# Kernel tuning notes

Hardware: AMD Instinct MI355X
Metric: run time of the kernel (lower is better)

The kernel has to match this reference:

```python
import jax, jax.numpy as jnp
import numpy as np

B, N_VAR, N_CLAUSE, K = 256, 10000, 40000, 3
N_NODE = N_VAR + N_CLAUSE


def setup_inputs() -> dict:
    key = jax.random.key(0)
    k1, k2, k3 = jax.random.split(key, 3)
    out = jax.random.normal(k1, (B, N_NODE), dtype=jnp.float32)
    # binary labels (torch y are 0/1 floats)
    y = (jax.random.uniform(k2, (B, N_NODE)) > 0.5).astype(jnp.float32)
    # mask: 0 on variable nodes, 1 on clause nodes
    mask = jnp.concatenate(
        [jnp.zeros((B, N_VAR), jnp.float32), jnp.ones((B, N_CLAUSE), jnp.float32)],
        axis=1,
    )
    # clauses: per graph, n_clause clauses of K variable indices in [0, n_var)
    clauses = jax.random.randint(k3, (B, N_CLAUSE, K), 0, N_VAR, dtype=jnp.int32)
    return {
        "out": out,
        "y": y,
        "mask": mask,
        "clauses": clauses,
        "n_var": N_VAR,
        "n_clause": N_CLAUSE,
    }


def _bce_with_logits(x, t):
    # elementwise BCE-with-logits: softplus(x) - x*t (numerically stable)
    return jax.nn.softplus(x) - x * t


def reference(out, y, mask, clauses, n_var, n_clause):
    b = out.shape[0]
    # loss 1: mean BCE over masked logits, divided by n_clause (per graph)
    loss1 = jnp.mean(_bce_with_logits(out * mask, y), axis=1) / n_clause  # [B]

    # hard predictions (detached in torch): sigmoid > 0.5, keep clause nodes only
    pred = (jax.nn.sigmoid(jax.lax.stop_gradient(out)) > 0.5).astype(out.dtype) * mask
    clause_active = pred[:, n_var:]  # [B, n_clause]

    # loadUnsatVariables: for each active clause, set its variables to 1.
    # Order-independent -> scatter-max of clause activation onto variable slots.
    flat_idx = (jnp.arange(b, dtype=jnp.int32)[:, None, None] * n_var
                + clauses).reshape(-1)  # [B*n_clause*K]
    vals = jnp.broadcast_to(clause_active[:, :, None], clauses.shape).reshape(-1)
    var_target = (jnp.zeros(b * n_var, out.dtype)
                  .at[flat_idx].max(vals)
                  .reshape(b, n_var))
    # target * (1 - mask): variable positions keep scatter result, clause part -> 0
    target = jnp.concatenate(
        [var_target, jnp.zeros((b, clause_active.shape[1]), out.dtype)], axis=1)

    loss2 = jnp.mean(_bce_with_logits(out * (1.0 - mask), target), axis=1) * 2.0
    return jnp.sum(loss1 + loss2)
```

## Files before the change

### kernel.cpp

```cpp
#include <hip/hip_runtime.h>

#define BB      256
#define NVAR    10000
#define NCLAUSE 40000
#define NNODE   50000
#define NT      1024


__device__ __forceinline__ float softplusf(float x) {
    return fmaxf(x, 0.f) + __logf(1.f + __expf(-fabsf(x)));
}

__global__ __launch_bounds__(NT) void k_fused(const float* __restrict__ outp,
                                              const float* __restrict__ yp,
                                              const int*   __restrict__ cl,
                                              float* __restrict__ accum) {
    __shared__ unsigned char flags[NVAR];
    __shared__ float red[NT / 64];
    const int b = blockIdx.x;
    const int tid = threadIdx.x;

    unsigned* fw = (unsigned*)flags;
    for (int i = tid; i < NVAR / 4; i += NT) fw[i] = 0u;
    __syncthreads();

    float s1 = 0.f;
    {
        const float* orow = outp + (size_t)b * NNODE + NVAR;
        const float* yrow = yp   + (size_t)b * NNODE + NVAR;
        const int*   crow = cl   + (size_t)b * NCLAUSE * 3;
        for (int t = tid; t < NCLAUSE / 4; t += NT) {
            const float4 o4 = *(const float4*)(orow + 4 * t);
            const float4 y4 = *(const float4*)(yrow + 4 * t);
            const int4* cp = (const int4*)(crow + 12 * t);
            const int4 c0 = cp[0], c1 = cp[1], c2 = cp[2];

            s1 += softplusf(o4.x) - o4.x * y4.x;
            s1 += softplusf(o4.y) - o4.y * y4.y;
            s1 += softplusf(o4.z) - o4.z * y4.z;
            s1 += softplusf(o4.w) - o4.w * y4.w;

            if (o4.x > 0.f) { flags[c0.x] = 1; flags[c0.y] = 1; flags[c0.z] = 1; }
            if (o4.y > 0.f) { flags[c0.w] = 1; flags[c1.x] = 1; flags[c1.y] = 1; }
            if (o4.z > 0.f) { flags[c1.z] = 1; flags[c1.w] = 1; flags[c2.x] = 1; }
            if (o4.w > 0.f) { flags[c2.y] = 1; flags[c2.z] = 1; flags[c2.w] = 1; }
        }
    }
    __syncthreads();

    float s2 = 0.f;
    {
        const float* vrow = outp + (size_t)b * NNODE;
        for (int t = tid; t < NVAR / 4; t += NT) {
            const float4 o4 = *(const float4*)(vrow + 4 * t);
            const unsigned f = fw[t];
            s2 += softplusf(o4.x) - o4.x * (float)( f        & 1u);
            s2 += softplusf(o4.y) - o4.y * (float)((f >> 8)  & 1u);
            s2 += softplusf(o4.z) - o4.z * (float)((f >> 16) & 1u);
            s2 += softplusf(o4.w) - o4.w * (float)((f >> 24) & 1u);
        }
    }

    float v = s1 * (1.0f / ((float)NNODE * (float)NCLAUSE)) + s2 * (2.0f / (float)NNODE);
    #pragma unroll
    for (int off = 32; off; off >>= 1) v += __shfl_down(v, off, 64);
    const int lane = tid & 63, w = tid >> 6;
    if (lane == 0) red[w] = v;
    __syncthreads();
    if (w == 0) {
        float r = (lane < NT / 64) ? red[lane] : 0.f;
        #pragma unroll
        for (int off = 8; off; off >>= 1) r += __shfl_down(r, off, 64);
        if (lane == 0) atomicAdd(accum, r);
    }
}

__global__ void k_fin(const float* __restrict__ accum, float* __restrict__ outp) {
    if (threadIdx.x == 0 && blockIdx.x == 0) {
        const double ln2 = 0.6931471805599453;
        double r = (double)accum[0]
                 + ((double)BB * NVAR * ln2) / ((double)NNODE * (double)NCLAUSE)
                 + 2.0 * ((double)BB * NCLAUSE * ln2) / (double)NNODE;
        outp[0] = (float)r;
    }
}

extern "C" void kernel_launch(void* const* d_in, const int* in_sizes, int n_in,
                              void* d_out, int out_size, void* d_ws, size_t ws_size,
                              hipStream_t stream) {
    const float* outp = (const float*)d_in[0];
    const float* yp   = (const float*)d_in[1];
    const int* cl     = (const int*)d_in[3];

    float* accum = (float*)d_ws;
    hipMemsetAsync(d_ws, 0, 16, stream);

    k_fused<<<BB, NT, 0, stream>>>(outp, yp, cl, accum);
    k_fin<<<1, 64, 0, stream>>>(accum, (float*)d_out);
}
```

Measured before the change: 43.60 us.

## Split clause scatter across two blocks per graph and add separate variable-loss kernel

```diff
diff --git a/kernel.cpp b/kernel.cpp
--- a/kernel.cpp
+++ b/kernel.cpp
@@ -4,32 +4,39 @@
 #define NVAR    10000
 #define NCLAUSE 40000
 #define NNODE   50000
-#define NT      1024
+#define NSPLIT  2
+#define NTA     1024
+#define NTB     512
+#define CL_PER_H (NCLAUSE / NSPLIT)
+#define V4_PER_H (CL_PER_H / 4)
+#define NWORDS   313
+#define LDSW     2504
 
 
 __device__ __forceinline__ float softplusf(float x) {
     return fmaxf(x, 0.f) + __logf(1.f + __expf(-fabsf(x)));
 }
 
-__global__ __launch_bounds__(NT) void k_fused(const float* __restrict__ outp,
-                                              const float* __restrict__ yp,
-                                              const int*   __restrict__ cl,
-                                              float* __restrict__ accum) {
-    __shared__ unsigned char flags[NVAR];
-    __shared__ float red[NT / 64];
-    const int b = blockIdx.x;
+__global__ __launch_bounds__(NTA) void k_clause(const float* __restrict__ outp,
+                                                const float* __restrict__ yp,
+                                                const int*   __restrict__ cl,
+                                                unsigned*    __restrict__ flagw,
+                                                float*       __restrict__ accum) {
+    __shared__ unsigned fw[LDSW];
+    __shared__ float red[NTA / 64];
+    const int b = blockIdx.y, h = blockIdx.x;
     const int tid = threadIdx.x;
 
-    unsigned* fw = (unsigned*)flags;
-    for (int i = tid; i < NVAR / 4; i += NT) fw[i] = 0u;
+    for (int i = tid; i < LDSW; i += NTA) fw[i] = 0u;
     __syncthreads();
 
+    unsigned char* flags = (unsigned char*)fw;
     float s1 = 0.f;
     {
-        const float* orow = outp + (size_t)b * NNODE + NVAR;
-        const float* yrow = yp   + (size_t)b * NNODE + NVAR;
-        const int*   crow = cl   + (size_t)b * NCLAUSE * 3;
-        for (int t = tid; t < NCLAUSE / 4; t += NT) {
+        const float* orow = outp + (size_t)b * NNODE + NVAR + h * CL_PER_H;
+        const float* yrow = yp   + (size_t)b * NNODE + NVAR + h * CL_PER_H;
+        const int*   crow = cl   + (size_t)b * NCLAUSE * 3 + (size_t)h * CL_PER_H * 3;
+        for (int t = tid; t < V4_PER_H; t += NTA) {
             const float4 o4 = *(const float4*)(orow + 4 * t);
             const float4 y4 = *(const float4*)(yrow + 4 * t);
             const int4* cp = (const int4*)(crow + 12 * t);
@@ -48,29 +55,67 @@
     }
     __syncthreads();
 
-    float s2 = 0.f;
-    {
-        const float* vrow = outp + (size_t)b * NNODE;
-        for (int t = tid; t < NVAR / 4; t += NT) {
-            const float4 o4 = *(const float4*)(vrow + 4 * t);
-            const unsigned f = fw[t];
-            s2 += softplusf(o4.x) - o4.x * (float)( f        & 1u);
-            s2 += softplusf(o4.y) - o4.y * (float)((f >> 8)  & 1u);
-            s2 += softplusf(o4.z) - o4.z * (float)((f >> 16) & 1u);
-            s2 += softplusf(o4.w) - o4.w * (float)((f >> 24) & 1u);
+    unsigned* dst = flagw + (size_t)(b * NSPLIT + h) * NWORDS;
+    for (int w = tid; w < NWORDS; w += NTA) {
+        unsigned r = 0;
+        #pragma unroll
+        for (int k = 0; k < 8; ++k) {
+            const unsigned u = fw[w * 8 + k];
+            const unsigned nib = (u | (u >> 7) | (u >> 14) | (u >> 21)) & 0xFu;
+            r |= nib << (4 * k);
         }
+        dst[w] = r;
     }
 
-    float v = s1 * (1.0f / ((float)NNODE * (float)NCLAUSE)) + s2 * (2.0f / (float)NNODE);
+    float v = s1 * (1.0f / ((float)NNODE * (float)NCLAUSE));
     #pragma unroll
     for (int off = 32; off; off >>= 1) v += __shfl_down(v, off, 64);
     const int lane = tid & 63, w = tid >> 6;
     if (lane == 0) red[w] = v;
     __syncthreads();
     if (w == 0) {
-        float r = (lane < NT / 64) ? red[lane] : 0.f;
+        float r = (lane < NTA / 64) ? red[lane] : 0.f;
         #pragma unroll
         for (int off = 8; off; off >>= 1) r += __shfl_down(r, off, 64);
+        if (lane == 0) atomicAdd(accum, r);
+    }
+}
+
+__global__ __launch_bounds__(NTB) void k_var(const float* __restrict__ outp,
+                                             const unsigned* __restrict__ flagw,
+                                             float* __restrict__ accum) {
+    __shared__ unsigned comb[NWORDS];
+    __shared__ float red[NTB / 64];
+    const int b = blockIdx.y, h = blockIdx.x;
+    const int tid = threadIdx.x;
+
+    const unsigned* p0 = flagw + (size_t)(b * NSPLIT + 0) * NWORDS;
+    const unsigned* p1 = flagw + (size_t)(b * NSPLIT + 1) * NWORDS;
+    for (int i = tid; i < NWORDS; i += NTB) comb[i] = p0[i] | p1[i];
+    __syncthreads();
+
+    float s2 = 0.f;
+    const float* vrow = outp + (size_t)b * NNODE + h * (NVAR / NSPLIT);
+    for (int t = tid; t < NVAR / NSPLIT / 4; t += NTB) {
+        const int vt = h * (NVAR / NSPLIT / 4) + t;
+        const float4 o4 = *(const float4*)(vrow + 4 * t);
+        const unsigned bits = (comb[vt >> 3] >> ((4 * vt) & 31)) & 0xFu;
+        s2 += softplusf(o4.x) - o4.x * (float)( bits       & 1u);
+        s2 += softplusf(o4.y) - o4.y * (float)((bits >> 1) & 1u);
+        s2 += softplusf(o4.z) - o4.z * (float)((bits >> 2) & 1u);
+        s2 += softplusf(o4.w) - o4.w * (float)((bits >> 3) & 1u);
+    }
+
+    float v = s2 * (2.0f / (float)NNODE);
+    #pragma unroll
+    for (int off = 32; off; off >>= 1) v += __shfl_down(v, off, 64);
+    const int lane = tid & 63, w = tid >> 6;
+    if (lane == 0) red[w] = v;
+    __syncthreads();
+    if (w == 0) {
+        float r = (lane < NTB / 64) ? red[lane] : 0.f;
+        #pragma unroll
+        for (int off = 4; off; off >>= 1) r += __shfl_down(r, off, 64);
         if (lane == 0) atomicAdd(accum, r);
     }
 }
@@ -93,8 +138,14 @@
     const int* cl     = (const int*)d_in[3];
 
     float* accum = (float*)d_ws;
+    unsigned* flagw = (unsigned*)((char*)d_ws + 16);
     hipMemsetAsync(d_ws, 0, 16, stream);
 
-    k_fused<<<BB, NT, 0, stream>>>(outp, yp, cl, accum);
+    dim3 gA(NSPLIT, BB);
+    k_clause<<<gA, NTA, 0, stream>>>(outp, yp, cl, flagw, accum);
+
+    dim3 gB(NSPLIT, BB);
+    k_var<<<gB, NTB, 0, stream>>>(outp, flagw, accum);
+
     k_fin<<<1, 64, 0, stream>>>(accum, (float*)d_out);
 }
```

After: 51.80 us. 18.8% more time.

## Software-pipeline clause loads, branchless flag stores, fold finalize into last block

Applied to the files above, without the earlier changes.

```diff
diff --git a/kernel.cpp b/kernel.cpp
--- a/kernel.cpp
+++ b/kernel.cpp
@@ -5,59 +5,81 @@
 #define NCLAUSE 40000
 #define NNODE   50000
 #define NT      1024
+#define NV4C    (NCLAUSE / 4)
+#define NV4V    (NVAR / 4)
+#define LDSW    2504
 
 
 __device__ __forceinline__ float softplusf(float x) {
     return fmaxf(x, 0.f) + __logf(1.f + __expf(-fabsf(x)));
 }
 
-__global__ __launch_bounds__(NT) void k_fused(const float* __restrict__ outp,
-                                              const float* __restrict__ yp,
-                                              const int*   __restrict__ cl,
-                                              float* __restrict__ accum) {
-    __shared__ unsigned char flags[NVAR];
+__global__ __launch_bounds__(NT) void k_all(const float* __restrict__ outp,
+                                            const float* __restrict__ yp,
+                                            const int*   __restrict__ cl,
+                                            float* __restrict__ accum,
+                                            unsigned* __restrict__ counter,
+                                            float* __restrict__ res) {
+    __shared__ unsigned fw[LDSW];
     __shared__ float red[NT / 64];
     const int b = blockIdx.x;
     const int tid = threadIdx.x;
+    unsigned char* flags = (unsigned char*)fw;
 
-    unsigned* fw = (unsigned*)flags;
-    for (int i = tid; i < NVAR / 4; i += NT) fw[i] = 0u;
+    for (int i = tid; i < LDSW; i += NT) fw[i] = 0u;
     __syncthreads();
 
+    const float* orow = outp + (size_t)b * NNODE + NVAR;
+    const float* yrow = yp   + (size_t)b * NNODE + NVAR;
+    const int*   crow = cl   + (size_t)b * NCLAUSE * 3;
+
     float s1 = 0.f;
-    {
-        const float* orow = outp + (size_t)b * NNODE + NVAR;
-        const float* yrow = yp   + (size_t)b * NNODE + NVAR;
-        const int*   crow = cl   + (size_t)b * NCLAUSE * 3;
-        for (int t = tid; t < NCLAUSE / 4; t += NT) {
-            const float4 o4 = *(const float4*)(orow + 4 * t);
-            const float4 y4 = *(const float4*)(yrow + 4 * t);
-            const int4* cp = (const int4*)(crow + 12 * t);
-            const int4 c0 = cp[0], c1 = cp[1], c2 = cp[2];
+    int t = tid;
+    bool valid = (t < NV4C);
+    float4 o4, y4; int4 c0, c1, c2;
+    if (valid) {
+        o4 = *(const float4*)(orow + 4 * t);
+        y4 = *(const float4*)(yrow + 4 * t);
+        const int4* cp = (const int4*)(crow + 12 * t);
+        c0 = cp[0]; c1 = cp[1]; c2 = cp[2];
+    }
+    while (valid) {
+        const int tn = t + NT;
+        const bool vn = (tn < NV4C);
+        float4 on, yn; int4 n0, n1, n2;
+        if (vn) {
+            on = *(const float4*)(orow + 4 * tn);
+            yn = *(const float4*)(yrow + 4 * tn);
+            const int4* cp = (const int4*)(crow + 12 * tn);
+            n0 = cp[0]; n1 = cp[1]; n2 = cp[2];
+        }
 
-            s1 += softplusf(o4.x) - o4.x * y4.x;
-            s1 += softplusf(o4.y) - o4.y * y4.y;
-            s1 += softplusf(o4.z) - o4.z * y4.z;
-            s1 += softplusf(o4.w) - o4.w * y4.w;
+        s1 += softplusf(o4.x) - o4.x * y4.x;
+        s1 += softplusf(o4.y) - o4.y * y4.y;
+        s1 += softplusf(o4.z) - o4.z * y4.z;
+        s1 += softplusf(o4.w) - o4.w * y4.w;
 
-            if (o4.x > 0.f) { flags[c0.x] = 1; flags[c0.y] = 1; flags[c0.z] = 1; }
-            if (o4.y > 0.f) { flags[c0.w] = 1; flags[c1.x] = 1; flags[c1.y] = 1; }
-            if (o4.z > 0.f) { flags[c1.z] = 1; flags[c1.w] = 1; flags[c2.x] = 1; }
-            if (o4.w > 0.f) { flags[c2.y] = 1; flags[c2.z] = 1; flags[c2.w] = 1; }
-        }
+        const bool ax = o4.x > 0.f, ay = o4.y > 0.f, az = o4.z > 0.f, aw = o4.w > 0.f;
+        flags[ax ? c0.x : NVAR] = 1; flags[ax ? c0.y : NVAR] = 1; flags[ax ? c0.z : NVAR] = 1;
+        flags[ay ? c0.w : NVAR] = 1; flags[ay ? c1.x : NVAR] = 1; flags[ay ? c1.y : NVAR] = 1;
+        flags[az ? c1.z : NVAR] = 1; flags[az ? c1.w : NVAR] = 1; flags[az ? c2.x : NVAR] = 1;
+        flags[aw ? c2.y : NVAR] = 1; flags[aw ? c2.z : NVAR] = 1; flags[aw ? c2.w : NVAR] = 1;
+
+        t = tn; valid = vn;
+        o4 = on; y4 = yn; c0 = n0; c1 = n1; c2 = n2;
     }
     __syncthreads();
 
     float s2 = 0.f;
     {
         const float* vrow = outp + (size_t)b * NNODE;
-        for (int t = tid; t < NVAR / 4; t += NT) {
-            const float4 o4 = *(const float4*)(vrow + 4 * t);
-            const unsigned f = fw[t];
-            s2 += softplusf(o4.x) - o4.x * (float)( f        & 1u);
-            s2 += softplusf(o4.y) - o4.y * (float)((f >> 8)  & 1u);
-            s2 += softplusf(o4.z) - o4.z * (float)((f >> 16) & 1u);
-            s2 += softplusf(o4.w) - o4.w * (float)((f >> 24) & 1u);
+        for (int v = tid; v < NV4V; v += NT) {
+            const float4 q4 = *(const float4*)(vrow + 4 * v);
+            const unsigned f = fw[v];
+            s2 += softplusf(q4.x) - q4.x * (float)( f        & 1u);
+            s2 += softplusf(q4.y) - q4.y * (float)((f >> 8)  & 1u);
+            s2 += softplusf(q4.z) - q4.z * (float)((f >> 16) & 1u);
+            s2 += softplusf(q4.w) - q4.w * (float)((f >> 24) & 1u);
         }
     }
 
@@ -67,21 +89,21 @@
     const int lane = tid & 63, w = tid >> 6;
     if (lane == 0) red[w] = v;
     __syncthreads();
-    if (w == 0) {
-        float r = (lane < NT / 64) ? red[lane] : 0.f;
+    if (tid == 0) {
+        float r = 0.f;
         #pragma unroll
-        for (int off = 8; off; off >>= 1) r += __shfl_down(r, off, 64);
-        if (lane == 0) atomicAdd(accum, r);
-    }
-}
-
-__global__ void k_fin(const float* __restrict__ accum, float* __restrict__ outp) {
-    if (threadIdx.x == 0 && blockIdx.x == 0) {
-        const double ln2 = 0.6931471805599453;
-        double r = (double)accum[0]
-                 + ((double)BB * NVAR * ln2) / ((double)NNODE * (double)NCLAUSE)
-                 + 2.0 * ((double)BB * NCLAUSE * ln2) / (double)NNODE;
-        outp[0] = (float)r;
+        for (int i = 0; i < NT / 64; ++i) r += red[i];
+        atomicAdd(accum, r);
+        __threadfence();
+        const unsigned old = atomicAdd(counter, 1u);
+        if (old == BB - 1) {
+            const float S = atomicAdd(accum, 0.0f);
+            const double ln2 = 0.6931471805599453;
+            double rr = (double)S
+                      + ((double)BB * NVAR * ln2) / ((double)NNODE * (double)NCLAUSE)
+                      + 2.0 * ((double)BB * NCLAUSE * ln2) / (double)NNODE;
+            res[0] = (float)rr;
+        }
     }
 }
 
@@ -93,8 +115,8 @@
     const int* cl     = (const int*)d_in[3];
 
     float* accum = (float*)d_ws;
+    unsigned* counter = (unsigned*)((char*)d_ws + 8);
     hipMemsetAsync(d_ws, 0, 16, stream);
 
-    k_fused<<<BB, NT, 0, stream>>>(outp, yp, cl, accum);
-    k_fin<<<1, 64, 0, stream>>>(accum, (float*)d_out);
+    k_all<<<BB, NT, 0, stream>>>(outp, yp, cl, accum, counter, (float*)d_out);
 }
```

Result: slower. 46.78 us (+7.3%).
